# Optimization experiments

Hardware: AMD Instinct MI355X
Metric: run time of the kernel (lower is better)

The kernel has to match this reference:

```python
import jax, jax.numpy as jnp
import numpy as np

D_MODEL = 1024
D_HIDDEN = 4096
NUM_EXPERT = 8
TOP_K = 2
B, N = 1, 8192


def setup_inputs() -> dict:
    key = jax.random.key(0)
    ks = jax.random.split(key, 8)
    s1 = 1.0 / np.sqrt(D_MODEL)
    s2 = 1.0 / np.sqrt(D_HIDDEN)
    return {
        "x": jax.random.normal(ks[0], (B, N, D_MODEL), jnp.float32),
        "expert_tokens": jax.random.normal(ks[1], (NUM_EXPERT, D_MODEL), jnp.float32),
        "W1": jax.random.normal(ks[2], (NUM_EXPERT, D_MODEL, D_HIDDEN), jnp.float32) * s1,
        "b1": jnp.zeros((NUM_EXPERT, D_HIDDEN), jnp.float32),
        "W2": jax.random.normal(ks[3], (NUM_EXPERT, D_HIDDEN, D_HIDDEN), jnp.float32) * s2,
        "b2": jnp.zeros((NUM_EXPERT, D_HIDDEN), jnp.float32),
        "W3": jax.random.normal(ks[4], (NUM_EXPERT, D_HIDDEN, D_MODEL), jnp.float32) * s2,
        "b3": jnp.zeros((NUM_EXPERT, D_MODEL), jnp.float32),
    }


def _expert_mlp(x, W1, b1, W2, b2, W3, b3):
    # Linear -> GELU (exact, matching torch nn.GELU) -> Linear -> GELU -> Linear
    h = jax.nn.gelu(jnp.einsum("bnd,dh->bnh", x, W1) + b1, approximate=False)
    h = jax.nn.gelu(jnp.einsum("bnh,hk->bnk", h, W2) + b2, approximate=False)
    return jnp.einsum("bnh,hd->bnd", h, W3) + b3


def reference(x, expert_tokens, W1, b1, W2, b2, W3, b3):
    # router scores: [B, N, E]
    scores = jnp.einsum("bnd,ed->bne", x, expert_tokens)
    _, topk_idx = jax.lax.top_k(scores, TOP_K)  # [B, N, TOP_K]
    outputs = jnp.zeros_like(x)
    num_expert = W1.shape[0]
    for i in range(num_expert):
        # gate weight = (# of top-k slots assigned to expert i) / top_k
        w = jnp.mean((topk_idx == i).astype(x.dtype), axis=-1, keepdims=True)
        y = _expert_mlp(x, W1[i], b1[i], W2[i], b2[i], W3[i], b3[i])
        outputs = outputs + y * w
    return outputs
```

## Files before the change

### kernel.cpp

```cpp
#include <hip/hip_runtime.h>
#include <stdint.h>

#define D_MODEL 1024
#define D_HID   4096
#define NEXP    8
#define NTOK    8192
#define TOTROW  (NTOK*2)

typedef unsigned short ushort_t;
typedef __attribute__((ext_vector_type(8))) short short8;
typedef __attribute__((ext_vector_type(4))) float f32x4;

static __device__ __forceinline__ ushort_t f2bf(float f) {
    union { float f; uint32_t u; } v; v.f = f;
    uint32_t u = v.u;
    uint32_t r = (u + 0x7FFFu + ((u >> 16) & 1u)) >> 16;
    return (ushort_t)r;
}
static __device__ __forceinline__ float bf2f(ushort_t h) {
    union { uint32_t u; float f; } v; v.u = ((uint32_t)h) << 16;
    return v.f;
}
static __device__ __forceinline__ float gelu_f(float x) {
    return 0.5f * x * (1.0f + erff(x * 0.70710678118654752f));
}

static __device__ __forceinline__ void gload_lds16(const void* g, void* l) {
    __builtin_amdgcn_global_load_lds(
        (const __attribute__((address_space(1))) void*)g,
        (__attribute__((address_space(3))) void*)l,
        16, 0, 0);
}

__global__ __launch_bounds__(256) void router_kernel(
    const float* __restrict__ x, const float* __restrict__ et,
    int* __restrict__ cnt, int* __restrict__ top2)
{
    __shared__ float lds_et[NEXP * D_MODEL];
    int t = threadIdx.x;
    #pragma unroll
    for (int i = 0; i < (NEXP * D_MODEL) / 256; ++i)
        lds_et[i * 256 + t] = et[i * 256 + t];
    __syncthreads();

    int lane = t & 63, wv = t >> 6;
    int n = blockIdx.x * 4 + wv;
    double s[NEXP];
    #pragma unroll
    for (int e = 0; e < NEXP; ++e) s[e] = 0.0;
    const float* xr = x + (size_t)n * D_MODEL;
    for (int it = 0; it < D_MODEL / 64; ++it) {
        float xv = xr[it * 64 + lane];
        #pragma unroll
        for (int e = 0; e < NEXP; ++e)
            s[e] += (double)(xv * lds_et[e * D_MODEL + it * 64 + lane]);
    }
    #pragma unroll
    for (int e = 0; e < NEXP; ++e)
        for (int off = 32; off; off >>= 1)
            s[e] += __shfl_xor(s[e], off);

    if (lane == 0) {
        int e1 = 0;
        for (int e = 1; e < NEXP; ++e) if (s[e] > s[e1]) e1 = e;
        int e2 = (e1 == 0) ? 1 : 0;
        for (int e = 0; e < NEXP; ++e) if (e != e1 && s[e] > s[e2]) e2 = e;
        top2[n * 2 + 0] = e1;
        top2[n * 2 + 1] = e2;
        atomicAdd(&cnt[e1], 1);
        atomicAdd(&cnt[e2], 1);
    }
}

__global__ void scan_kernel(const int* __restrict__ cnt, int* __restrict__ base,
                            int* __restrict__ cnt2)
{
    if (threadIdx.x == 0 && blockIdx.x == 0) {
        int acc = 0;
        for (int e = 0; e < NEXP; ++e) { base[e] = acc; acc += cnt[e]; cnt2[e] = 0; }
    }
}

__global__ __launch_bounds__(256) void assign_kernel(
    const int* __restrict__ top2, const int* __restrict__ base,
    int* __restrict__ cnt2, int* __restrict__ rowinfo, int* __restrict__ token_rows)
{
    int n = blockIdx.x * 256 + threadIdx.x;
    if (n >= NTOK) return;
    #pragma unroll
    for (int k = 0; k < 2; ++k) {
        int e = top2[n * 2 + k];
        int slot = atomicAdd(&cnt2[e], 1);
        int row = base[e] + slot;
        rowinfo[row] = n;
        token_rows[n * 2 + k] = row;
    }
}

__global__ __launch_bounds__(256) void convert_x(
    const float* __restrict__ x, ushort_t* __restrict__ xb)
{
    size_t i = ((size_t)blockIdx.x * 256 + threadIdx.x) * 4;
    float4 f = *(const float4*)(x + i);
    ushort_t o[4];
    o[0] = f2bf(f.x); o[1] = f2bf(f.y); o[2] = f2bf(f.z); o[3] = f2bf(f.w);
    *(uint2*)(xb + i) = *(const uint2*)o;
}

__global__ __launch_bounds__(256) void transpose_kernel(
    const float* __restrict__ in, ushort_t* __restrict__ out, int K, int N)
{
    __shared__ float tile[64][65];
    int e = blockIdx.z;
    int k0 = blockIdx.y * 64, n0 = blockIdx.x * 64;
    const float* ine = in + (size_t)e * K * N + (size_t)k0 * N + n0;
    ushort_t* oute = out + (size_t)e * N * K + (size_t)n0 * K + k0;
    int t = threadIdx.x;
    int lr = t >> 4;
    int lc = (t & 15) * 4;
    #pragma unroll
    for (int i = 0; i < 4; ++i) {
        float4 v = *(const float4*)(ine + (size_t)(i * 16 + lr) * N + lc);
        tile[i * 16 + lr][lc + 0] = v.x;
        tile[i * 16 + lr][lc + 1] = v.y;
        tile[i * 16 + lr][lc + 2] = v.z;
        tile[i * 16 + lr][lc + 3] = v.w;
    }
    __syncthreads();
    int nr = t >> 3;
    int kg = (t & 7) * 8;
    #pragma unroll
    for (int j = 0; j < 2; ++j) {
        int n = j * 32 + nr;
        ushort_t o[8];
        #pragma unroll
        for (int m = 0; m < 8; ++m) o[m] = f2bf(tile[kg + m][n]);
        *(uint4*)(oute + (size_t)n * K + kg) = *(const uint4*)o;
    }
}


#define RD_A(BUF, MH) do {                                                        \
    _Pragma("unroll") for (int mi = 0; mi < 4; ++mi) {                            \
        areg[mi][0] = *(const short8*)(pA0 + (BUF)*16384 + (MH)*4096 + mi*1024);  \
        areg[mi][1] = *(const short8*)(pA1 + (BUF)*16384 + (MH)*4096 + mi*1024);  \
    }                                                                             \
} while (0)

#define RD_B(DST, BUF, NH) do {                                                   \
    _Pragma("unroll") for (int ni = 0; ni < 2; ++ni) {                            \
        DST[ni][0] = *(const short8*)(pB0 + (BUF)*16384 + (NH)*2048 + ni*1024);   \
        DST[ni][1] = *(const short8*)(pB1 + (BUF)*16384 + (NH)*2048 + ni*1024);   \
    }                                                                             \
} while (0)

#define MM(BR, MH, NH) do {                                                       \
    __builtin_amdgcn_s_setprio(1);                                                \
    _Pragma("unroll") for (int mi = 0; mi < 4; ++mi)                              \
    _Pragma("unroll") for (int ni = 0; ni < 2; ++ni)                              \
    _Pragma("unroll") for (int ks = 0; ks < 2; ++ks)                              \
      acc[(MH)*4 + mi][(NH)*2 + ni] = __builtin_amdgcn_mfma_f32_16x16x32_bf16(    \
          areg[mi][ks], BR[ni][ks], acc[(MH)*4 + mi][(NH)*2 + ni], 0, 0, 0);      \
    __builtin_amdgcn_s_setprio(0);                                                \
} while (0)

#define PH(MH, NH, BR, TAIL) do { MM(BR, MH, NH); TAIL; __builtin_amdgcn_s_barrier(); } while (0)

#define VW6 asm volatile("s_waitcnt vmcnt(6)" ::: "memory")
#define VW0 asm volatile("s_waitcnt vmcnt(0)" ::: "memory")

template<bool GATHER, bool GELU_ACT>
__global__ __launch_bounds__(512, 2) void moe_gemm8(
    const ushort_t* __restrict__ Ah,
    const ushort_t* __restrict__ BT,
    const float* __restrict__ bias,
    ushort_t* __restrict__ C,
    const int* __restrict__ cnt, const int* __restrict__ basep,
    const int* __restrict__ rowinfo,
    int Ncols, int K)
{
    const int e = blockIdx.z;
    const int cnte = cnt[e];
    const int mt = blockIdx.y;
    if (mt * 256 >= cnte) return;
    const int base_e = basep[e];
    const int row0 = base_e + mt * 256;
    const int col0 = blockIdx.x * 256;

    __shared__ __attribute__((aligned(16))) ushort_t SMEM[2][2][256][64];

    const int t = threadIdx.x;
    const int lane = t & 63;
    const int wv = t >> 6;
    const int wm = wv >> 2;
    const int wn = wv & 3;
    const int l15 = lane & 15, lhi = lane >> 4;
    const int key = l15 & 7;
    const int lr8 = lane >> 3;
    const int sl  = (lane & 7) ^ lr8;

    const int slot0 = (lhi ^ key) * 8;
    const int slot1 = ((4 + lhi) ^ key) * 8;
    const ushort_t* pA0 = &SMEM[0][0][wm * 128 + l15][slot0];
    const ushort_t* pA1 = &SMEM[0][0][wm * 128 + l15][slot1];
    const ushort_t* pB0 = &SMEM[1][0][wn * 64 + l15][slot0];
    const ushort_t* pB1 = &SMEM[1][0][wn * 64 + l15][slot1];

    uint32_t aOff[2][2], bOff[2][2];
    #pragma unroll
    for (int mh = 0; mh < 2; ++mh)
        #pragma unroll
        for (int c = 0; c < 2; ++c) {
            int tr = mh * 64 + wv * 8 + lr8 + c * 128;
            int gr = row0 + tr; if (gr > TOTROW - 1) gr = TOTROW - 1;
            uint32_t rowid = GATHER ? (uint32_t)rowinfo[gr] : (uint32_t)gr;
            aOff[mh][c] = rowid * (uint32_t)(K * 2) + sl * 16;
        }
    #pragma unroll
    for (int nh = 0; nh < 2; ++nh)
        #pragma unroll
        for (int c = 0; c < 2; ++c) {
            int tr = (wv >> 2) * 64 + nh * 32 + (wv & 3) * 8 + lr8 + c * 128;
            bOff[nh][c] = ((uint32_t)e * Ncols + col0 + tr) * (uint32_t)(K * 2) + sl * 16;
        }

    const int arb = wv * 8;
    const int brb = (wv >> 2) * 64 + (wv & 3) * 8;

    auto stageA = [&](int buf, int mh) {
        gload_lds16((const char*)Ah + aOff[mh][0], (void*)&SMEM[0][buf][mh * 64 + arb][0]);
        gload_lds16((const char*)Ah + aOff[mh][1], (void*)&SMEM[0][buf][128 + mh * 64 + arb][0]);
        aOff[mh][0] += 128; aOff[mh][1] += 128;
    };
    auto stageB = [&](int buf, int nh) {
        gload_lds16((const char*)BT + bOff[nh][0], (void*)&SMEM[1][buf][nh * 32 + brb][0]);
        gload_lds16((const char*)BT + bOff[nh][1], (void*)&SMEM[1][buf][128 + nh * 32 + brb][0]);
        bOff[nh][0] += 128; bOff[nh][1] += 128;
    };

    f32x4 acc[8][4];
    #pragma unroll
    for (int i = 0; i < 8; ++i)
        #pragma unroll
        for (int j = 0; j < 4; ++j)
            acc[i][j] = (f32x4){0.f, 0.f, 0.f, 0.f};

    short8 areg[4][2], breg0[2][2], breg1[2][2];

    const int KT = K / 64;
    const int NIT = KT / 2;

    stageA(0, 0); stageB(0, 0); stageB(0, 1); stageA(0, 1);
    stageA(1, 0); stageB(1, 0); stageB(1, 1); stageA(1, 1);
    VW0;
    __builtin_amdgcn_s_barrier();
    RD_A(0, 0); RD_B(breg0, 0, 0);

    for (int i2 = 0; i2 < NIT - 1; ++i2) {
         PH(0, 0, breg0, { stageA(0, 0); RD_B(breg1, 0, 1); });
         PH(0, 1, breg1, { stageB(0, 0); RD_A(0, 1); });
         PH(1, 1, breg1, { stageB(0, 1); VW6; });
         PH(1, 0, breg0, { stageA(0, 1); RD_A(1, 0); RD_B(breg0, 1, 0); });
         PH(0, 0, breg0, { stageA(1, 0); RD_B(breg1, 1, 1); });
         PH(0, 1, breg1, { stageB(1, 0); RD_A(1, 1); });
         PH(1, 1, breg1, { stageB(1, 1); VW6; });
         PH(1, 0, breg0, { stageA(1, 1); RD_A(0, 0); RD_B(breg0, 0, 0); });
    }
    {
         PH(0, 0, breg0, { RD_B(breg1, 0, 1); });
         PH(0, 1, breg1, { RD_A(0, 1); });
         PH(1, 1, breg1, { VW0; });
         PH(1, 0, breg0, { RD_A(1, 0); RD_B(breg0, 1, 0); });
         PH(0, 0, breg0, { RD_B(breg1, 1, 1); });
         PH(0, 1, breg1, { RD_A(1, 1); });
         PH(1, 1, breg1, { });
         MM(breg0, 1, 0);
    }

    ushort_t* ctile = &SMEM[0][0][0][0];
    #pragma unroll
    for (int n = 0; n < 4; ++n) {
        int c = wn * 64 + n * 16 + l15;
        float bv = bias[e * Ncols + col0 + c];
        #pragma unroll
        for (int m = 0; m < 8; ++m) {
            #pragma unroll
            for (int q = 0; q < 4; ++q) {
                int r = wm * 128 + m * 16 + lhi * 4 + q;
                float v = acc[m][n][q] + bv;
                if (GELU_ACT) v = gelu_f(v);
                ctile[r * 256 + ((c >> 3) ^ ((r & 7) << 2)) * 8 + (c & 7)] = f2bf(v);
            }
        }
    }
    __syncthreads();
    {
        int rr = t >> 2;
        int ch0 = t & 3;
        #pragma unroll
        for (int pass = 0; pass < 2; ++pass) {
            int r = pass * 128 + rr;
            int rl = mt * 256 + r;
            if (rl < cnte) {
                size_t gbase = (size_t)(base_e + rl) * Ncols + col0;
                #pragma unroll
                for (int i = 0; i < 8; ++i) {
                    int ch = ch0 + i * 4;
                    uint4 v = *(const uint4*)&ctile[r * 256 + ((ch ^ ((r & 7) << 2)) * 8)];
                    *(uint4*)&C[gbase + ch * 8] = v;
                }
            }
        }
    }
}

__global__ __launch_bounds__(256) void combine_kernel(
    const ushort_t* __restrict__ Y, const int* __restrict__ token_rows,
    float* __restrict__ out)
{
    int n = blockIdx.x;
    int t = threadIdx.x;
    int r1 = token_rows[n * 2 + 0], r2 = token_rows[n * 2 + 1];
    const ushort_t* y1 = Y + (size_t)r1 * D_MODEL + t * 4;
    const ushort_t* y2 = Y + (size_t)r2 * D_MODEL + t * 4;
    ushort_t a[4], b[4];
    *(uint2*)a = *(const uint2*)y1;
    *(uint2*)b = *(const uint2*)y2;
    float4 o;
    o.x = 0.5f * (bf2f(a[0]) + bf2f(b[0]));
    o.y = 0.5f * (bf2f(a[1]) + bf2f(b[1]));
    o.z = 0.5f * (bf2f(a[2]) + bf2f(b[2]));
    o.w = 0.5f * (bf2f(a[3]) + bf2f(b[3]));
    *(float4*)(out + (size_t)n * D_MODEL + t * 4) = o;
}

extern "C" void kernel_launch(void* const* d_in, const int* in_sizes, int n_in,
                              void* d_out, int out_size, void* d_ws, size_t ws_size,
                              hipStream_t stream)
{
    const float* x  = (const float*)d_in[0];
    const float* et = (const float*)d_in[1];
    const float* W1 = (const float*)d_in[2];
    const float* b1 = (const float*)d_in[3];
    const float* W2 = (const float*)d_in[4];
    const float* b2 = (const float*)d_in[5];
    const float* W3 = (const float*)d_in[6];
    const float* b3 = (const float*)d_in[7];
    float* out = (float*)d_out;

    char* ws = (char*)d_ws;
    size_t off = 0;
    auto alloc = [&](size_t bytes) -> char* {
        char* p = ws + off;
        off += (bytes + 255) & ~(size_t)255;
        return p;
    };
    int* cnt        = (int*)alloc(NEXP * 4);
    int* basep      = (int*)alloc(NEXP * 4);
    int* cnt2       = (int*)alloc(NEXP * 4);
    int* top2       = (int*)alloc((size_t)NTOK * 2 * 4);
    int* token_rows = (int*)alloc((size_t)NTOK * 2 * 4);
    int* rowinfo    = (int*)alloc((size_t)TOTROW * 4);
    ushort_t* W1T = (ushort_t*)alloc((size_t)NEXP * D_HID * D_MODEL * 2);
    ushort_t* W2T = (ushort_t*)alloc((size_t)NEXP * D_HID * D_HID * 2);
    ushort_t* W3T = (ushort_t*)alloc((size_t)NEXP * D_MODEL * D_HID * 2);
    ushort_t* H1  = (ushort_t*)alloc((size_t)TOTROW * D_HID * 2);
    ushort_t* H2  = (ushort_t*)alloc((size_t)TOTROW * D_HID * 2);
    ushort_t* Yr  = (ushort_t*)alloc((size_t)TOTROW * D_MODEL * 2);
    if (off > ws_size) return;

    ushort_t* xb = H2;

    hipMemsetAsync(cnt, 0, NEXP * 4, stream);
    router_kernel<<<NTOK / 4, 256, 0, stream>>>(x, et, cnt, top2);
    scan_kernel<<<1, 64, 0, stream>>>(cnt, basep, cnt2);
    assign_kernel<<<NTOK / 256, 256, 0, stream>>>(top2, basep, cnt2, rowinfo, token_rows);

    convert_x<<<(NTOK * D_MODEL) / 1024, 256, 0, stream>>>(x, xb);

    transpose_kernel<<<dim3(D_HID / 64, D_MODEL / 64, NEXP), 256, 0, stream>>>(W1, W1T, D_MODEL, D_HID);
    transpose_kernel<<<dim3(D_HID / 64, D_HID / 64, NEXP), 256, 0, stream>>>(W2, W2T, D_HID, D_HID);
    transpose_kernel<<<dim3(D_MODEL / 64, D_HID / 64, NEXP), 256, 0, stream>>>(W3, W3T, D_HID, D_MODEL);

    moe_gemm8<true, true><<<dim3(D_HID / 256, 16, NEXP), 512, 0, stream>>>(
        xb, W1T, b1, H1, cnt, basep, rowinfo, D_HID, D_MODEL);
    moe_gemm8<false, true><<<dim3(D_HID / 256, 16, NEXP), 512, 0, stream>>>(
        H1, W2T, b2, H2, cnt, basep, rowinfo, D_HID, D_HID);
    moe_gemm8<false, false><<<dim3(D_MODEL / 256, 16, NEXP), 512, 0, stream>>>(
        H2, W3T, b3, Yr, cnt, basep, rowinfo, D_MODEL, D_HID);

    combine_kernel<<<NTOK, 256, 0, stream>>>(Yr, token_rows, out);
}
```

Before: 1.502 ms.

## Switch MoE GEMM to 32x32x16 MFMA and fuse bf16 x conversion into router

The grouped expert GEMM now uses 32x32x16 bf16 MFMA tiles instead of 16x16x32, with the LDS read addressing, register fragments and epilogue row mapping reworked to match. Larger MFMA tiles need fewer LDS fragment reads per FLOP and fewer instructions issued. Separately, the router kernel now writes the bf16 copy of x while it reads x, which removes the standalone convert_x kernel and one extra pass over x. The risks are higher accumulator register pressure and possible LDS bank conflicts under the new swizzle pattern.

New measurement: 1.577 ms. +5.0%, slower.

```diff
diff --git a/kernel.cpp b/kernel.cpp
--- a/kernel.cpp
+++ b/kernel.cpp
@@ -9,7 +9,7 @@
 
 typedef unsigned short ushort_t;
 typedef __attribute__((ext_vector_type(8))) short short8;
-typedef __attribute__((ext_vector_type(4))) float f32x4;
+typedef __attribute__((ext_vector_type(16))) float f32x16;
 
 static __device__ __forceinline__ ushort_t f2bf(float f) {
     union { float f; uint32_t u; } v; v.f = f;
@@ -34,7 +34,7 @@
 
 __global__ __launch_bounds__(256) void router_kernel(
     const float* __restrict__ x, const float* __restrict__ et,
-    int* __restrict__ cnt, int* __restrict__ top2)
+    int* __restrict__ cnt, int* __restrict__ top2, ushort_t* __restrict__ xb)
 {
     __shared__ float lds_et[NEXP * D_MODEL];
     int t = threadIdx.x;
@@ -49,8 +49,10 @@
     #pragma unroll
     for (int e = 0; e < NEXP; ++e) s[e] = 0.0;
     const float* xr = x + (size_t)n * D_MODEL;
+    ushort_t* xbr = xb + (size_t)n * D_MODEL;
     for (int it = 0; it < D_MODEL / 64; ++it) {
         float xv = xr[it * 64 + lane];
+        xbr[it * 64 + lane] = f2bf(xv);
         #pragma unroll
         for (int e = 0; e < NEXP; ++e)
             s[e] += (double)(xv * lds_et[e * D_MODEL + it * 64 + lane]);
@@ -97,16 +99,6 @@
     }
 }
 
-__global__ __launch_bounds__(256) void convert_x(
-    const float* __restrict__ x, ushort_t* __restrict__ xb)
-{
-    size_t i = ((size_t)blockIdx.x * 256 + threadIdx.x) * 4;
-    float4 f = *(const float4*)(x + i);
-    ushort_t o[4];
-    o[0] = f2bf(f.x); o[1] = f2bf(f.y); o[2] = f2bf(f.z); o[3] = f2bf(f.w);
-    *(uint2*)(xb + i) = *(const uint2*)o;
-}
-
 __global__ __launch_bounds__(256) void transpose_kernel(
     const float* __restrict__ in, ushort_t* __restrict__ out, int K, int N)
 {
@@ -140,31 +132,27 @@
 }
 
 
-#define RD_A(BUF, MH) do {                                                        \
-    _Pragma("unroll") for (int mi = 0; mi < 4; ++mi) {                            \
-        areg[mi][0] = *(const short8*)(pA0 + (BUF)*16384 + (MH)*4096 + mi*1024);  \
-        areg[mi][1] = *(const short8*)(pA1 + (BUF)*16384 + (MH)*4096 + mi*1024);  \
-    }                                                                             \
+#define RD_A32(BUF, MH) do {                                                       \
+    _Pragma("unroll") for (int mi2 = 0; mi2 < 2; ++mi2)                            \
+    _Pragma("unroll") for (int ks = 0; ks < 4; ++ks)                               \
+        areg[mi2][ks] = *(const short8*)(pAk[ks] + (BUF)*16384 + (MH)*4096 + mi2*2048); \
 } while (0)
 
-#define RD_B(DST, BUF, NH) do {                                                   \
-    _Pragma("unroll") for (int ni = 0; ni < 2; ++ni) {                            \
-        DST[ni][0] = *(const short8*)(pB0 + (BUF)*16384 + (NH)*2048 + ni*1024);   \
-        DST[ni][1] = *(const short8*)(pB1 + (BUF)*16384 + (NH)*2048 + ni*1024);   \
-    }                                                                             \
+#define RD_B32(DST, BUF, NH) do {                                                  \
+    _Pragma("unroll") for (int ks = 0; ks < 4; ++ks)                               \
+        DST[ks] = *(const short8*)(pBk[ks] + (BUF)*16384 + (NH)*2048);             \
 } while (0)
 
-#define MM(BR, MH, NH) do {                                                       \
-    __builtin_amdgcn_s_setprio(1);                                                \
-    _Pragma("unroll") for (int mi = 0; mi < 4; ++mi)                              \
-    _Pragma("unroll") for (int ni = 0; ni < 2; ++ni)                              \
-    _Pragma("unroll") for (int ks = 0; ks < 2; ++ks)                              \
-      acc[(MH)*4 + mi][(NH)*2 + ni] = __builtin_amdgcn_mfma_f32_16x16x32_bf16(    \
-          areg[mi][ks], BR[ni][ks], acc[(MH)*4 + mi][(NH)*2 + ni], 0, 0, 0);      \
-    __builtin_amdgcn_s_setprio(0);                                                \
+#define MM32(BR, MH, NH) do {                                                      \
+    __builtin_amdgcn_s_setprio(1);                                                 \
+    _Pragma("unroll") for (int mi2 = 0; mi2 < 2; ++mi2)                            \
+    _Pragma("unroll") for (int ks = 0; ks < 4; ++ks)                               \
+      acc32[(MH)*2 + mi2][NH] = __builtin_amdgcn_mfma_f32_32x32x16_bf16(           \
+          areg[mi2][ks], BR[ks], acc32[(MH)*2 + mi2][NH], 0, 0, 0);                \
+    __builtin_amdgcn_s_setprio(0);                                                 \
 } while (0)
 
-#define PH(MH, NH, BR, TAIL) do { MM(BR, MH, NH); TAIL; __builtin_amdgcn_s_barrier(); } while (0)
+#define PH32(MH, NH, BR, TAIL) do { MM32(BR, MH, NH); TAIL; __builtin_amdgcn_s_barrier(); } while (0)
 
 #define VW6 asm volatile("s_waitcnt vmcnt(6)" ::: "memory")
 #define VW0 asm volatile("s_waitcnt vmcnt(0)" ::: "memory")
@@ -194,17 +182,19 @@
     const int wv = t >> 6;
     const int wm = wv >> 2;
     const int wn = wv & 3;
-    const int l15 = lane & 15, lhi = lane >> 4;
-    const int key = l15 & 7;
+    const int l31 = lane & 31, l5 = lane >> 5;
+    const int key = lane & 7;
     const int lr8 = lane >> 3;
     const int sl  = (lane & 7) ^ lr8;
 
-    const int slot0 = (lhi ^ key) * 8;
-    const int slot1 = ((4 + lhi) ^ key) * 8;
-    const ushort_t* pA0 = &SMEM[0][0][wm * 128 + l15][slot0];
-    const ushort_t* pA1 = &SMEM[0][0][wm * 128 + l15][slot1];
-    const ushort_t* pB0 = &SMEM[1][0][wn * 64 + l15][slot0];
-    const ushort_t* pB1 = &SMEM[1][0][wn * 64 + l15][slot1];
+    const ushort_t* pAk[4];
+    const ushort_t* pBk[4];
+    #pragma unroll
+    for (int ks = 0; ks < 4; ++ks) {
+        int so = ((ks * 2 + l5) ^ key) * 8;
+        pAk[ks] = &SMEM[0][0][wm * 128 + l31][0] + so;
+        pBk[ks] = &SMEM[1][0][wn * 64 + l31][0] + so;
+    }
 
     uint32_t aOff[2][2], bOff[2][2];
     #pragma unroll
@@ -238,14 +228,16 @@
         bOff[nh][0] += 128; bOff[nh][1] += 128;
     };
 
-    f32x4 acc[8][4];
-    #pragma unroll
-    for (int i = 0; i < 8; ++i)
-        #pragma unroll
-        for (int j = 0; j < 4; ++j)
-            acc[i][j] = (f32x4){0.f, 0.f, 0.f, 0.f};
-
-    short8 areg[4][2], breg0[2][2], breg1[2][2];
+    f32x16 acc32[4][2];
+    #pragma unroll
+    for (int i = 0; i < 4; ++i)
+        #pragma unroll
+        for (int j = 0; j < 2; ++j)
+            #pragma unroll
+            for (int r = 0; r < 16; ++r)
+                acc32[i][j][r] = 0.f;
+
+    short8 areg[2][4], breg0[4], breg1[4];
 
     const int KT = K / 64;
     const int NIT = KT / 2;
@@ -254,42 +246,42 @@
     stageA(1, 0); stageB(1, 0); stageB(1, 1); stageA(1, 1);
     VW0;
     __builtin_amdgcn_s_barrier();
-    RD_A(0, 0); RD_B(breg0, 0, 0);
+    RD_A32(0, 0); RD_B32(breg0, 0, 0);
 
     for (int i2 = 0; i2 < NIT - 1; ++i2) {
-         PH(0, 0, breg0, { stageA(0, 0); RD_B(breg1, 0, 1); });
-         PH(0, 1, breg1, { stageB(0, 0); RD_A(0, 1); });
-         PH(1, 1, breg1, { stageB(0, 1); VW6; });
-         PH(1, 0, breg0, { stageA(0, 1); RD_A(1, 0); RD_B(breg0, 1, 0); });
-         PH(0, 0, breg0, { stageA(1, 0); RD_B(breg1, 1, 1); });
-         PH(0, 1, breg1, { stageB(1, 0); RD_A(1, 1); });
-         PH(1, 1, breg1, { stageB(1, 1); VW6; });
-         PH(1, 0, breg0, { stageA(1, 1); RD_A(0, 0); RD_B(breg0, 0, 0); });
+         PH32(0, 0, breg0, { stageA(0, 0); RD_B32(breg1, 0, 1); });
+         PH32(0, 1, breg1, { stageB(0, 0); RD_A32(0, 1); });
+         PH32(1, 1, breg1, { stageB(0, 1); VW6; });
+         PH32(1, 0, breg0, { stageA(0, 1); RD_A32(1, 0); RD_B32(breg0, 1, 0); });
+         PH32(0, 0, breg0, { stageA(1, 0); RD_B32(breg1, 1, 1); });
+         PH32(0, 1, breg1, { stageB(1, 0); RD_A32(1, 1); });
+         PH32(1, 1, breg1, { stageB(1, 1); VW6; });
+         PH32(1, 0, breg0, { stageA(1, 1); RD_A32(0, 0); RD_B32(breg0, 0, 0); });
     }
     {
-         PH(0, 0, breg0, { RD_B(breg1, 0, 1); });
-         PH(0, 1, breg1, { RD_A(0, 1); });
-         PH(1, 1, breg1, { VW0; });
-         PH(1, 0, breg0, { RD_A(1, 0); RD_B(breg0, 1, 0); });
-         PH(0, 0, breg0, { RD_B(breg1, 1, 1); });
-         PH(0, 1, breg1, { RD_A(1, 1); });
-         PH(1, 1, breg1, { });
-         MM(breg0, 1, 0);
+         PH32(0, 0, breg0, { RD_B32(breg1, 0, 1); });
+         PH32(0, 1, breg1, { RD_A32(0, 1); });
+         PH32(1, 1, breg1, { VW0; });
+         PH32(1, 0, breg0, { RD_A32(1, 0); RD_B32(breg0, 1, 0); });
+         PH32(0, 0, breg0, { RD_B32(breg1, 1, 1); });
+         PH32(0, 1, breg1, { RD_A32(1, 1); });
+         PH32(1, 1, breg1, { });
+         MM32(breg0, 1, 0);
     }
 
     ushort_t* ctile = &SMEM[0][0][0][0];
     #pragma unroll
-    for (int n = 0; n < 4; ++n) {
-        int c = wn * 64 + n * 16 + l15;
+    for (int nt = 0; nt < 2; ++nt) {
+        int c = wn * 64 + nt * 32 + l31;
         float bv = bias[e * Ncols + col0 + c];
         #pragma unroll
-        for (int m = 0; m < 8; ++m) {
+        for (int mtl = 0; mtl < 4; ++mtl) {
             #pragma unroll
-            for (int q = 0; q < 4; ++q) {
-                int r = wm * 128 + m * 16 + lhi * 4 + q;
-                float v = acc[m][n][q] + bv;
+            for (int r = 0; r < 16; ++r) {
+                int row = wm * 128 + mtl * 32 + (r & 3) + 8 * (r >> 2) + 4 * l5;
+                float v = acc32[mtl][nt][r] + bv;
                 if (GELU_ACT) v = gelu_f(v);
-                ctile[r * 256 + ((c >> 3) ^ ((r & 7) << 2)) * 8 + (c & 7)] = f2bf(v);
+                ctile[row * 256 + ((c >> 3) ^ ((row & 7) << 2)) * 8 + (c & 7)] = f2bf(v);
             }
         }
     }
@@ -372,11 +364,9 @@
     ushort_t* xb = H2;
 
     hipMemsetAsync(cnt, 0, NEXP * 4, stream);
-    router_kernel<<<NTOK / 4, 256, 0, stream>>>(x, et, cnt, top2);
+    router_kernel<<<NTOK / 4, 256, 0, stream>>>(x, et, cnt, top2, xb);
     scan_kernel<<<1, 64, 0, stream>>>(cnt, basep, cnt2);
     assign_kernel<<<NTOK / 256, 256, 0, stream>>>(top2, basep, cnt2, rowinfo, token_rows);
-
-    convert_x<<<(NTOK * D_MODEL) / 1024, 256, 0, stream>>>(x, xb);
 
     transpose_kernel<<<dim3(D_HID / 64, D_MODEL / 64, NEXP), 256, 0, stream>>>(W1, W1T, D_MODEL, D_HID);
     transpose_kernel<<<dim3(D_HID / 64, D_HID / 64, NEXP), 256, 0, stream>>>(W2, W2T, D_HID, D_HID);
```
